# Kernel tuning notes

Hardware: AMD Instinct MI355X
Metric: run time of the kernel (lower is better)

## Reference

```python
import jax, jax.numpy as jnp
import numpy as np

N, E, C, S, G = 20000, 320000, 32, 64, 64
NRAD, HRAD, OUTS, HHEAD, NSH, NL = 8, 64, 16, 64, 9, 2
RCUT = 5.0
LIDX = np.repeat(np.arange(3), [1, 3, 5])  # l index of each of the 9 sh components


def _sph_harm(u):
    # real spherical harmonics up to l=2 on unit vectors, [E,3] -> [E,9]
    x, y, z = u[:, 0], u[:, 1], u[:, 2]
    s3 = jnp.sqrt(jnp.asarray(3.0, u.dtype))
    return jnp.stack([
        jnp.ones_like(x), x, y, z,
        s3 * x * y, s3 * y * z, 0.5 * (3 * z * z - 1.0), s3 * x * z,
        0.5 * s3 * (x * x - y * y)
    ], axis=1)


def _bessel(r):
    # Bessel radial basis with smooth polynomial envelope, [E] -> [E, NRAD]
    n = jnp.arange(1, NRAD + 1, dtype=r.dtype)
    rs = jnp.clip(r, 1e-6, None)[:, None]
    u = jnp.clip(r / RCUT, 0.0, 1.0)
    env = ((1 - u) ** 2 * (1 + 2 * u))[:, None]
    return jnp.sqrt(2.0 / RCUT) * jnp.sin(n * jnp.pi * rs / RCUT) / rs * env


def setup_inputs() -> dict:
    key = jax.random.key(0)
    ks = jax.random.split(key, 16)
    return {
        'vectors': jax.random.normal(ks[0], (E, 3), jnp.float32),
        'node_species': jax.random.randint(ks[1], (N,), 0, S),
        'senders': jax.random.randint(ks[2], (E,), 0, N),
        'receivers': jax.random.randint(ks[3], (E,), 0, N),
        'graph_id': jnp.sort(jax.random.randint(ks[4], (N,), 0, G)),
        'species_embed': jax.random.normal(ks[5], (S, C), jnp.float32) * 0.1,
        'w_r1': jax.random.normal(ks[6], (NRAD, HRAD), jnp.float32) / np.sqrt(NRAD),
        'b_r1': jnp.zeros((HRAD,), jnp.float32),
        'w_r2': jax.random.normal(ks[7], (NL, HRAD, 3 * C), jnp.float32) / np.sqrt(HRAD),
        'w_mix': jax.random.normal(ks[8], (NL, 3, C, C), jnp.float32) / np.sqrt(C),
        'w_sc': jax.random.normal(ks[9], (NL, S, C, C), jnp.float32) / np.sqrt(C),
        'w_readout': jax.random.normal(ks[10], (C, OUTS), jnp.float32) / np.sqrt(C),
        'ln_gamma': jnp.ones((OUTS,), jnp.float32),
        'ln_beta': jnp.zeros((OUTS,), jnp.float32),
        'w_h1': jax.random.normal(ks[11], (OUTS, HHEAD), jnp.float32) / np.sqrt(OUTS),
        'b_h1': jnp.zeros((HHEAD,), jnp.float32),
        'w_h2': jax.random.normal(ks[12], (HHEAD, 1), jnp.float32) / np.sqrt(HHEAD),
        'b_h2': jnp.zeros((1,), jnp.float32),
        'scale': jnp.ones((), jnp.float32),
        'shift': jnp.zeros((), jnp.float32),
    }


def reference(vectors, node_species, senders, receivers, graph_id, species_embed,
              w_r1, b_r1, w_r2, w_mix, w_sc, w_readout, ln_gamma, ln_beta,
              w_h1, b_h1, w_h2, b_h2, scale, shift):
    lidx = jnp.asarray(LIDX)
    # nan-safe edge norms and unit vectors (safe_norm in source)
    r2 = jnp.sum(vectors ** 2, axis=-1)
    r = jnp.where(r2 == 0, 0.0, jnp.sqrt(jnp.where(r2 == 0, 1.0, r2)))
    u = vectors / jnp.where(r == 0, 1.0, r)[:, None]
    sh = _sph_harm(u)                                  # [E,9]
    rad = jax.nn.silu(_bessel(r) @ w_r1 + b_r1)        # [E,HRAD] radial MLP
    h = species_embed[node_species]                    # [N,C] node embedding
    for li in range(NL):
        # per-edge, per-l, per-channel radial weights, expanded to the 9 sh components
        rw = (rad @ w_r2[li]).reshape(E, 3, C)[:, lidx, :]     # [E,9,C]
        # tensor-product message: radial * sender scalars * Y_lm
        msg = sh[:, :, None] * rw * h[senders][:, None, :]     # [E,9,C]
        agg = jax.ops.segment_sum(msg, receivers, num_segments=N)  # [N,9,C]
        # per-irrep (per-l) channel-mixing linear
        mixed = jnp.einsum('nmc,mcd->nmd', agg, w_mix[li][lidx])   # [N,9,C]
        # species-dependent self-connection on the scalar (l=0) channel
        sc = jnp.einsum('nc,ncd->nd', h, w_sc[li][node_species])   # [N,C]
        h = mixed[:, 0, :] + sc + h                                # residual
    readout = h @ w_readout                            # [N,OUTS] (last-block readout)
    mu = jnp.mean(readout, axis=-1, keepdims=True)
    var = jnp.var(readout, axis=-1, keepdims=True)
    nrm = (readout - mu) * jax.lax.rsqrt(var + 1e-6) * ln_gamma + ln_beta
    node_out = (jax.nn.gelu(nrm @ w_h1 + b_h1) @ w_h2 + b_h2)[:, 0]  # [N]
    gsum = jax.ops.segment_sum(node_out, graph_id, num_segments=G)
    cnt = jax.ops.segment_sum(jnp.ones((N,), node_out.dtype), graph_id, num_segments=G)
    gmean = gsum / jnp.clip(cnt, 1.0, None)            # segment-mean node2graph
    return (gmean * scale + shift)[:, None]            # [G,1]
```

## Files before the change

### kernel.cpp

```cpp
#include <hip/hip_runtime.h>
#include <hip/hip_fp16.h>
#include <cstdint>
#include <cmath>

#define NE 320000
#define NN 20000
#define NG 64

typedef __attribute__((ext_vector_type(8))) short s16x8;
typedef __attribute__((ext_vector_type(4))) float f32x4;

static __device__ __forceinline__ unsigned short f32_to_bf16(float x) {
    unsigned int u = __float_as_uint(x);
    u = (u + 0x7fffu + ((u >> 16) & 1u)) >> 16;
    return (unsigned short)u;
}
static __device__ __forceinline__ float bf16_to_f32(unsigned short h) {
    return __uint_as_float(((unsigned int)h) << 16);
}

__global__ __launch_bounds__(256) void setup_kernel(
    const int* __restrict__ spec, const float* __restrict__ emb,
    float* __restrict__ h,
    const float* __restrict__ w_r2,
    unsigned short* __restrict__ wt_hi, unsigned short* __restrict__ wt_lo,
    int* __restrict__ deg, float* __restrict__ gz)
{
    int t = blockIdx.x * 256 + threadIdx.x;
    if (t < NN * 32) h[t] = emb[spec[t >> 5] * 32 + (t & 31)];
    if (t < 4096) {
        int c = t >> 6, k = t & 63;
        float v = w_r2[(c >= 32 ? 6144 : 0) + k * 96 + (c & 31)];
        unsigned short hb = f32_to_bf16(v);
        wt_hi[t] = hb;
        wt_lo[t] = f32_to_bf16(v - bf16_to_f32(hb));
    }
    if (t < NN) deg[t] = 0;
    if (t < 128) gz[t] = 0.0f;
}

__global__ __launch_bounds__(256) void count_kernel(
    const int* __restrict__ recv, int* __restrict__ deg)
{
    int e = blockIdx.x * 256 + threadIdx.x;
    atomicAdd(&deg[recv[e]], 1);
}

__global__ __launch_bounds__(1024) void scan_kernel(
    const int* __restrict__ deg,
    int* __restrict__ rowstart, int* __restrict__ cursor)
{
    __shared__ int tsum[1024];
    const int tid = threadIdx.x;
    const int PER = (NN + 1023) / 1024;
    const int base = tid * PER;

    int s = 0;
    for (int i = 0; i < PER; ++i) {
        int idx = base + i;
        if (idx < NN) s += deg[idx];
    }
    tsum[tid] = s;
    __syncthreads();
    for (int off = 1; off < 1024; off <<= 1) {
        int v = (tid >= off) ? tsum[tid - off] : 0;
        __syncthreads();
        tsum[tid] += v;
        __syncthreads();
    }
    int run = tsum[tid] - s;
    for (int i = 0; i < PER; ++i) {
        int idx = base + i;
        if (idx < NN) {
            rowstart[idx] = run;
            cursor[idx] = run;
            run += deg[idx];
        }
    }
    if (tid == 1023) rowstart[NN] = NE;
}

__global__ __launch_bounds__(256) void scatter_kernel(
    const int* __restrict__ recv, const int* __restrict__ snd,
    int* __restrict__ cursor, int* __restrict__ eperm, int* __restrict__ esnd)
{
    int e = blockIdx.x * 256 + threadIdx.x;
    int slot = atomicAdd(&cursor[recv[e]], 1);
    eperm[e] = slot;
    esnd[slot] = snd[e];
}

__global__ __launch_bounds__(256) void edge_gemm_kernel(
    const float* __restrict__ vectors,
    const float* __restrict__ w_r1,
    const float* __restrict__ b_r1,
    const unsigned short* __restrict__ wt_hi,
    const unsigned short* __restrict__ wt_lo,
    const int* __restrict__ eperm,
    __half* __restrict__ rw0_0,
    __half* __restrict__ rw0_1)
{
    __shared__ __attribute__((aligned(16))) short sh_hi[256 * 72];
    __shared__ __attribute__((aligned(16))) short sh_lo[256 * 72];

    const int tid = threadIdx.x;
    const int e = blockIdx.x * 256 + tid;
    const int slot = eperm[e];

    float x = vectors[3 * e + 0];
    float y = vectors[3 * e + 1];
    float z = vectors[3 * e + 2];
    float r2 = x * x + y * y + z * z;
    float r = (r2 == 0.0f) ? 0.0f : sqrtf(r2);
    float rs = fmaxf(r, 1e-6f);
    float u = fminf(r * 0.2f, 1.0f);
    float env = (1.0f - u) * (1.0f - u) * (1.0f + 2.0f * u);
    float pref = 0.6324555320336759f * env / rs;
    float theta = 0.6283185307179586f * rs;

    float s1 = __sinf(theta), c1 = __cosf(theta);
    float twoc = 2.0f * c1;
    float b[8];
    {
        float sp = 0.0f, s = s1;
#pragma unroll
        for (int n = 0; n < 8; ++n) {
            b[n] = pref * s;
            float nx = twoc * s - sp;
            sp = s; s = nx;
        }
    }

#pragma unroll
    for (int j0 = 0; j0 < 64; j0 += 8) {
        short hibuf[8], lobuf[8];
#pragma unroll
        for (int jj = 0; jj < 8; ++jj) {
            int j = j0 + jj;
            float pre = b_r1[j];
#pragma unroll
            for (int n = 0; n < 8; ++n) pre = fmaf(b[n], w_r1[n * 64 + j], pre);
            float rj = pre * __builtin_amdgcn_rcpf(1.0f + __expf(-pre));
            unsigned short hb = f32_to_bf16(rj);
            float lov = rj - bf16_to_f32(hb);
            hibuf[jj] = (short)hb;
            lobuf[jj] = (short)f32_to_bf16(lov);
        }
        *(s16x8*)&sh_hi[tid * 72 + j0] =
            (s16x8){hibuf[0],hibuf[1],hibuf[2],hibuf[3],hibuf[4],hibuf[5],hibuf[6],hibuf[7]};
        *(s16x8*)&sh_lo[tid * 72 + j0] =
            (s16x8){lobuf[0],lobuf[1],lobuf[2],lobuf[3],lobuf[4],lobuf[5],lobuf[6],lobuf[7]};
    }

    __syncthreads();

    const int wv = tid >> 6;
    const int l = tid & 63;
    const int lrow = l & 15;
    const int lk = l >> 4;

    s16x8 Bhi[4][2], Blo[4][2];
#pragma unroll
    for (int ct = 0; ct < 4; ++ct)
#pragma unroll
        for (int kt = 0; kt < 2; ++kt) {
            int col = ct * 16 + lrow;
            int kof = kt * 32 + lk * 8;
            Bhi[ct][kt] = *(const s16x8*)(wt_hi + col * 64 + kof);
            Blo[ct][kt] = *(const s16x8*)(wt_lo + col * 64 + kof);
        }

    f32x4 acc[4][4];
#pragma unroll
    for (int rt = 0; rt < 4; ++rt)
#pragma unroll
        for (int ct = 0; ct < 4; ++ct) acc[rt][ct] = (f32x4){0.f, 0.f, 0.f, 0.f};

#pragma unroll
    for (int rt = 0; rt < 4; ++rt) {
        int row = wv * 64 + rt * 16 + lrow;
#pragma unroll
        for (int kt = 0; kt < 2; ++kt) {
            s16x8 ahi = *(const s16x8*)&sh_hi[row * 72 + kt * 32 + lk * 8];
            s16x8 alo = *(const s16x8*)&sh_lo[row * 72 + kt * 32 + lk * 8];
#pragma unroll
            for (int ct = 0; ct < 4; ++ct) {
                acc[rt][ct] = __builtin_amdgcn_mfma_f32_16x16x32_bf16(ahi, Bhi[ct][kt], acc[rt][ct], 0, 0, 0);
                acc[rt][ct] = __builtin_amdgcn_mfma_f32_16x16x32_bf16(alo, Bhi[ct][kt], acc[rt][ct], 0, 0, 0);
                acc[rt][ct] = __builtin_amdgcn_mfma_f32_16x16x32_bf16(ahi, Blo[ct][kt], acc[rt][ct], 0, 0, 0);
            }
        }
    }

    __syncthreads();
    __half* stg = (__half*)sh_hi;
#pragma unroll
    for (int rt = 0; rt < 4; ++rt)
#pragma unroll
        for (int ct = 0; ct < 4; ++ct) {
            int col = ct * 16 + lrow;
#pragma unroll
            for (int rr = 0; rr < 4; ++rr) {
                int erow = wv * 64 + rt * 16 + lk * 4 + rr;
                stg[erow * 72 + col] = __float2half_rn(acc[rt][ct][rr]);
            }
        }
    __syncthreads();
    {
        const s16x8* src = (const s16x8*)&sh_hi[tid * 72];
        size_t eb = (size_t)slot * 32;
        s16x8* d0 = (s16x8*)(rw0_0 + eb);
        s16x8* d1 = (s16x8*)(rw0_1 + eb);
        d0[0] = src[0]; d0[1] = src[1]; d0[2] = src[2]; d0[3] = src[3];
        d1[0] = src[4]; d1[1] = src[5]; d1[2] = src[6]; d1[3] = src[7];
    }
}

__device__ __forceinline__ float agg_update_val(
    const __half* __restrict__ rw0h, const float* __restrict__ hin,
    const int* __restrict__ rowstart, const int* __restrict__ esnd,
    const int* __restrict__ spec,
    const float* __restrict__ wmix0, const float* __restrict__ wscl,
    int t, int n, int c, int half)
{
    int s0 = rowstart[n], s1 = rowstart[n + 1];
    float hv = hin[t];

    float p0 = 0.f, p1 = 0.f, p2 = 0.f, p3 = 0.f;
    int k = s0;
    for (; k + 4 <= s1; k += 4) {
        int sA = esnd[k], sB = esnd[k + 1], sC = esnd[k + 2], sD = esnd[k + 3];
        float rA = __half2float(rw0h[(size_t)k * 32 + c]);
        float rB = __half2float(rw0h[(size_t)(k + 1) * 32 + c]);
        float rC = __half2float(rw0h[(size_t)(k + 2) * 32 + c]);
        float rD = __half2float(rw0h[(size_t)(k + 3) * 32 + c]);
        float hA = hin[(size_t)sA * 32 + c];
        float hB = hin[(size_t)sB * 32 + c];
        float hC = hin[(size_t)sC * 32 + c];
        float hD = hin[(size_t)sD * 32 + c];
        p0 = fmaf(rA, hA, p0);
        p1 = fmaf(rB, hB, p1);
        p2 = fmaf(rC, hC, p2);
        p3 = fmaf(rD, hD, p3);
    }
    for (; k < s1; ++k)
        p0 = fmaf(__half2float(rw0h[(size_t)k * 32 + c]),
                  hin[(size_t)esnd[k] * 32 + c], p0);
    float acc = (p0 + p1) + (p2 + p3);

    const float* wsc = wscl + spec[n] * 1024;
    float m0 = 0.f, m1 = 0.f, q0 = 0.f, q1 = 0.f;
#pragma unroll
    for (int cp = 0; cp < 32; cp += 2) {
        float av0 = __shfl(acc, half + cp);
        float hb0 = __shfl(hv, half + cp);
        float av1 = __shfl(acc, half + cp + 1);
        float hb1 = __shfl(hv, half + cp + 1);
        m0 = fmaf(av0, wmix0[cp * 32 + c], m0);
        q0 = fmaf(hb0, wsc[cp * 32 + c], q0);
        m1 = fmaf(av1, wmix0[(cp + 1) * 32 + c], m1);
        q1 = fmaf(hb1, wsc[(cp + 1) * 32 + c], q1);
    }
    return hv + (m0 + m1) + (q0 + q1);
}

__global__ __launch_bounds__(256) void agg_update_kernel(
    const __half* __restrict__ rw0h, const float* __restrict__ hin,
    const int* __restrict__ rowstart, const int* __restrict__ esnd,
    const int* __restrict__ spec,
    const float* __restrict__ wmix0, const float* __restrict__ wscl,
    float* __restrict__ hout)
{
    int t = blockIdx.x * 256 + threadIdx.x;
    int n = t >> 5, c = t & 31;
    int half = (threadIdx.x & 63) & 32;
    hout[t] = agg_update_val(rw0h, hin, rowstart, esnd, spec, wmix0, wscl,
                             t, n, c, half);
}

__global__ __launch_bounds__(256) void agg_readout_kernel(
    const __half* __restrict__ rw0h, const float* __restrict__ hin,
    const int* __restrict__ rowstart, const int* __restrict__ esnd,
    const int* __restrict__ spec,
    const float* __restrict__ wmix0, const float* __restrict__ wscl,
    const int* __restrict__ gid_arr,
    const float* __restrict__ w_ro,
    const float* __restrict__ gamma, const float* __restrict__ beta,
    const float* __restrict__ w_h1, const float* __restrict__ b_h1,
    const float* __restrict__ w_h2, const float* __restrict__ b_h2,
    float* __restrict__ gsum, float* __restrict__ gcnt)
{
    __shared__ int sgid[8];
    __shared__ float sval[8];

    int t = blockIdx.x * 256 + threadIdx.x;
    int n = t >> 5, c = t & 31;
    int half = (threadIdx.x & 63) & 32;

    float outv = agg_update_val(rw0h, hin, rowstart, esnd, spec, wmix0, wscl,
                                t, n, c, half);

    int o = c & 15;
    float r0 = 0.f, r1 = 0.f, r2 = 0.f, r3 = 0.f;
#pragma unroll
    for (int cp = 0; cp < 32; cp += 4) {
        r0 = fmaf(__shfl(outv, half + cp),     w_ro[cp * 16 + o],       r0);
        r1 = fmaf(__shfl(outv, half + cp + 1), w_ro[(cp + 1) * 16 + o], r1);
        r2 = fmaf(__shfl(outv, half + cp + 2), w_ro[(cp + 2) * 16 + o], r2);
        r3 = fmaf(__shfl(outv, half + cp + 3), w_ro[(cp + 3) * 16 + o], r3);
    }
    float ro = (r0 + r1) + (r2 + r3);

    float ssum = ro;
#pragma unroll
    for (int m = 1; m < 16; m <<= 1) ssum += __shfl_xor(ssum, m);
    float mu = ssum * (1.0f / 16.0f);
    float d = ro - mu;
    float vs = d * d;
#pragma unroll
    for (int m = 1; m < 16; m <<= 1) vs += __shfl_xor(vs, m);
    float inv = rsqrtf(vs * (1.0f / 16.0f) + 1e-6f);
    float nrm = d * inv * gamma[o] + beta[o];

    int j1 = c, j2 = c + 32;
    float a1a = b_h1[j1], a1b = 0.f, a2a = b_h1[j2], a2b = 0.f;
#pragma unroll
    for (int oo = 0; oo < 16; oo += 2) {
        float nv0 = __shfl(nrm, half + oo);
        float nv1 = __shfl(nrm, half + oo + 1);
        a1a = fmaf(nv0, w_h1[oo * 64 + j1], a1a);
        a2a = fmaf(nv0, w_h1[oo * 64 + j2], a2a);
        a1b = fmaf(nv1, w_h1[(oo + 1) * 64 + j1], a1b);
        a2b = fmaf(nv1, w_h1[(oo + 1) * 64 + j2], a2b);
    }
    float a1 = a1a + a1b, a2 = a2a + a2b;
    float g1 = 0.5f * a1 * (1.0f + tanhf(0.7978845608028654f * (a1 + 0.044715f * a1 * a1 * a1)));
    float g2 = 0.5f * a2 * (1.0f + tanhf(0.7978845608028654f * (a2 + 0.044715f * a2 * a2 * a2)));
    float partial = fmaf(g1, w_h2[j1], g2 * w_h2[j2]);
#pragma unroll
    for (int m = 1; m < 32; m <<= 1) partial += __shfl_xor(partial, m);

    if (c == 0) {
        int hw = threadIdx.x >> 5;
        sgid[hw] = gid_arr[n];
        sval[hw] = partial + b_h2[0];
    }
    __syncthreads();
    if (threadIdx.x == 0) {
        int g0 = sgid[0];
        float accv = sval[0];
        float cnt = 1.0f;
        for (int i = 1; i < 8; ++i) {
            if (sgid[i] == g0) { accv += sval[i]; cnt += 1.0f; }
            else {
                atomicAdd(&gsum[g0], accv);
                atomicAdd(&gcnt[g0], cnt);
                g0 = sgid[i]; accv = sval[i]; cnt = 1.0f;
            }
        }
        atomicAdd(&gsum[g0], accv);
        atomicAdd(&gcnt[g0], cnt);
    }
}

__global__ void finalize_kernel(const float* __restrict__ gsum,
                                const float* __restrict__ gcnt,
                                const float* __restrict__ scale,
                                const float* __restrict__ shift,
                                float* __restrict__ out)
{
    int g = threadIdx.x;
    if (g < NG) out[g] = gsum[g] / fmaxf(gcnt[g], 1.0f) * scale[0] + shift[0];
}

extern "C" void kernel_launch(void* const* d_in, const int* in_sizes, int n_in,
                              void* d_out, int out_size, void* d_ws, size_t ws_size,
                              hipStream_t stream)
{
    const float* vectors       = (const float*)d_in[0];
    const int*   node_species  = (const int*)d_in[1];
    const int*   senders       = (const int*)d_in[2];
    const int*   receivers     = (const int*)d_in[3];
    const int*   graph_id      = (const int*)d_in[4];
    const float* species_embed = (const float*)d_in[5];
    const float* w_r1          = (const float*)d_in[6];
    const float* b_r1          = (const float*)d_in[7];
    const float* w_r2          = (const float*)d_in[8];
    const float* w_mix         = (const float*)d_in[9];
    const float* w_sc          = (const float*)d_in[10];
    const float* w_ro          = (const float*)d_in[11];
    const float* ln_gamma      = (const float*)d_in[12];
    const float* ln_beta       = (const float*)d_in[13];
    const float* w_h1          = (const float*)d_in[14];
    const float* b_h1          = (const float*)d_in[15];
    const float* w_h2          = (const float*)d_in[16];
    const float* b_h2          = (const float*)d_in[17];
    const float* scale         = (const float*)d_in[18];
    const float* shift         = (const float*)d_in[19];
    float* out = (float*)d_out;

    __half* rw0_0 = (__half*)d_ws;
    __half* rw0_1 = rw0_0 + (size_t)NE * 32;
    float* hA     = (float*)(rw0_1 + (size_t)NE * 32);
    float* hB     = hA + (size_t)NN * 32;
    float* gsum   = hB + (size_t)NN * 32;
    float* gcnt   = gsum + NG;
    unsigned short* wt_hi = (unsigned short*)(gcnt + NG);
    unsigned short* wt_lo = wt_hi + 4096;
    int* deg      = (int*)(wt_lo + 4096);
    int* rowstart = deg + NN;
    int* cursor   = rowstart + NN + 1;
    int* eperm    = cursor + NN + 1;
    int* esnd     = eperm + NE;

    setup_kernel<<<(NN * 32 + 255) / 256, 256, 0, stream>>>(
        node_species, species_embed, hA, w_r2, wt_hi, wt_lo, deg, gsum);

    count_kernel<<<NE / 256, 256, 0, stream>>>(receivers, deg);

    scan_kernel<<<1, 1024, 0, stream>>>(deg, rowstart, cursor);

    scatter_kernel<<<NE / 256, 256, 0, stream>>>(receivers, senders, cursor, eperm, esnd);

    edge_gemm_kernel<<<NE / 256, 256, 0, stream>>>(
        vectors, w_r1, b_r1, wt_hi, wt_lo, eperm, rw0_0, rw0_1);

    agg_update_kernel<<<(NN * 32) / 256, 256, 0, stream>>>(
        rw0_0, hA, rowstart, esnd, node_species, w_mix, w_sc, hB);

    agg_readout_kernel<<<(NN * 32) / 256, 256, 0, stream>>>(
        rw0_1, hB, rowstart, esnd, node_species, w_mix + 3072, w_sc + 65536,
        graph_id, w_ro, ln_gamma, ln_beta, w_h1, b_h1, w_h2, b_h2, gsum, gcnt);

    finalize_kernel<<<1, 64, 0, stream>>>(gsum, gcnt, scale, shift, out);
}
```

Measured before the change: 174.7 us.

## Fuse count+scan and readout+finalize via last-block tickets; gather edge GEMM by slot

Merges the degree-count and prefix-scan kernels into one launch in which the last block to finish does the scan, found with an atomic ticket. Finalize is folded into the readout kernel the same way. The scatter now records an inverse permutation, so the edge GEMM runs in CSR slot order: it gathers the input vectors and writes its outputs contiguously. GELU's tanh form is rewritten through exp and a fast reciprocal. The aim is fewer launches and coalesced edge writes, at the cost of a single-block serial scan tail, scattered reads of the vectors, and a slight change in GELU accuracy.

```diff
diff --git a/kernel.cpp b/kernel.cpp
--- a/kernel.cpp
+++ b/kernel.cpp
@@ -21,13 +21,13 @@
 
 __global__ __launch_bounds__(256) void setup_kernel(
     const int* __restrict__ spec, const float* __restrict__ emb,
-    float* __restrict__ h,
+    float* __restrict__ hA,
     const float* __restrict__ w_r2,
     unsigned short* __restrict__ wt_hi, unsigned short* __restrict__ wt_lo,
-    int* __restrict__ deg, float* __restrict__ gz)
+    int* __restrict__ deg, float* __restrict__ gz, int* __restrict__ tickets)
 {
     int t = blockIdx.x * 256 + threadIdx.x;
-    if (t < NN * 32) h[t] = emb[spec[t >> 5] * 32 + (t & 31)];
+    if (t < NN * 32) hA[t] = emb[spec[t >> 5] * 32 + (t & 31)];
     if (t < 4096) {
         int c = t >> 6, k = t & 63;
         float v = w_r2[(c >= 32 ? 6144 : 0) + k * 96 + (c & 31)];
@@ -37,24 +37,27 @@
     }
     if (t < NN) deg[t] = 0;
     if (t < 128) gz[t] = 0.0f;
-}
-
-__global__ __launch_bounds__(256) void count_kernel(
-    const int* __restrict__ recv, int* __restrict__ deg)
-{
-    int e = blockIdx.x * 256 + threadIdx.x;
-    atomicAdd(&deg[recv[e]], 1);
-}
-
-__global__ __launch_bounds__(1024) void scan_kernel(
-    const int* __restrict__ deg,
-    int* __restrict__ rowstart, int* __restrict__ cursor)
-{
+    if (t < 2) tickets[t] = 0;
+}
+
+__global__ __launch_bounds__(1024) void count_scan_kernel(
+    const int* __restrict__ recv,
+    int* __restrict__ deg, int* __restrict__ rowstart, int* __restrict__ cursor,
+    int* __restrict__ ticket)
+{
+    __shared__ int is_last;
     __shared__ int tsum[1024];
     const int tid = threadIdx.x;
-    const int PER = (NN + 1023) / 1024;
+    int e = blockIdx.x * 1024 + tid;
+    if (e < NE) atomicAdd(&deg[recv[e]], 1);
+    __threadfence();
+    __syncthreads();
+    if (tid == 0) is_last = (atomicAdd(ticket, 1) == (int)gridDim.x - 1);
+    __syncthreads();
+    if (!is_last) return;
+
+    const int PER = 20;
     const int base = tid * PER;
-
     int s = 0;
     for (int i = 0; i < PER; ++i) {
         int idx = base + i;
@@ -82,11 +85,11 @@
 
 __global__ __launch_bounds__(256) void scatter_kernel(
     const int* __restrict__ recv, const int* __restrict__ snd,
-    int* __restrict__ cursor, int* __restrict__ eperm, int* __restrict__ esnd)
+    int* __restrict__ cursor, int* __restrict__ eidp, int* __restrict__ esnd)
 {
     int e = blockIdx.x * 256 + threadIdx.x;
     int slot = atomicAdd(&cursor[recv[e]], 1);
-    eperm[e] = slot;
+    eidp[slot] = e;
     esnd[slot] = snd[e];
 }
 
@@ -96,7 +99,7 @@
     const float* __restrict__ b_r1,
     const unsigned short* __restrict__ wt_hi,
     const unsigned short* __restrict__ wt_lo,
-    const int* __restrict__ eperm,
+    const int* __restrict__ eidp,
     __half* __restrict__ rw0_0,
     __half* __restrict__ rw0_1)
 {
@@ -104,8 +107,8 @@
     __shared__ __attribute__((aligned(16))) short sh_lo[256 * 72];
 
     const int tid = threadIdx.x;
-    const int e = blockIdx.x * 256 + tid;
-    const int slot = eperm[e];
+    const int slot = blockIdx.x * 256 + tid;
+    const int e = eidp[slot];
 
     float x = vectors[3 * e + 0];
     float y = vectors[3 * e + 1];
@@ -208,9 +211,9 @@
     __syncthreads();
     {
         const s16x8* src = (const s16x8*)&sh_hi[tid * 72];
-        size_t eb = (size_t)slot * 32;
-        s16x8* d0 = (s16x8*)(rw0_0 + eb);
-        s16x8* d1 = (s16x8*)(rw0_1 + eb);
+        size_t sb = (size_t)slot * 32;
+        s16x8* d0 = (s16x8*)(rw0_0 + sb);
+        s16x8* d1 = (s16x8*)(rw0_1 + sb);
         d0[0] = src[0]; d0[1] = src[1]; d0[2] = src[2]; d0[3] = src[3];
         d1[0] = src[4]; d1[1] = src[5]; d1[2] = src[6]; d1[3] = src[7];
     }
@@ -288,10 +291,14 @@
     const float* __restrict__ gamma, const float* __restrict__ beta,
     const float* __restrict__ w_h1, const float* __restrict__ b_h1,
     const float* __restrict__ w_h2, const float* __restrict__ b_h2,
-    float* __restrict__ gsum, float* __restrict__ gcnt)
+    float* __restrict__ gsum, float* __restrict__ gcnt,
+    int* __restrict__ ticket,
+    const float* __restrict__ scale, const float* __restrict__ shift,
+    float* __restrict__ out)
 {
     __shared__ int sgid[8];
     __shared__ float sval[8];
+    __shared__ int is_last;
 
     int t = blockIdx.x * 256 + threadIdx.x;
     int n = t >> 5, c = t & 31;
@@ -334,8 +341,10 @@
         a2b = fmaf(nv1, w_h1[(oo + 1) * 64 + j2], a2b);
     }
     float a1 = a1a + a1b, a2 = a2a + a2b;
-    float g1 = 0.5f * a1 * (1.0f + tanhf(0.7978845608028654f * (a1 + 0.044715f * a1 * a1 * a1)));
-    float g2 = 0.5f * a2 * (1.0f + tanhf(0.7978845608028654f * (a2 + 0.044715f * a2 * a2 * a2)));
+    float g1 = a1 * __builtin_amdgcn_rcpf(
+        1.0f + __expf(-1.5957691216057308f * (a1 + 0.044715f * a1 * a1 * a1)));
+    float g2 = a2 * __builtin_amdgcn_rcpf(
+        1.0f + __expf(-1.5957691216057308f * (a2 + 0.044715f * a2 * a2 * a2)));
     float partial = fmaf(g1, w_h2[j1], g2 * w_h2[j2]);
 #pragma unroll
     for (int m = 1; m < 32; m <<= 1) partial += __shfl_xor(partial, m);
@@ -361,16 +370,16 @@
         atomicAdd(&gsum[g0], accv);
         atomicAdd(&gcnt[g0], cnt);
     }
-}
-
-__global__ void finalize_kernel(const float* __restrict__ gsum,
-                                const float* __restrict__ gcnt,
-                                const float* __restrict__ scale,
-                                const float* __restrict__ shift,
-                                float* __restrict__ out)
-{
-    int g = threadIdx.x;
-    if (g < NG) out[g] = gsum[g] / fmaxf(gcnt[g], 1.0f) * scale[0] + shift[0];
+
+    __threadfence();
+    __syncthreads();
+    if (threadIdx.x == 0) is_last = (atomicAdd(ticket, 1) == (int)gridDim.x - 1);
+    __syncthreads();
+    if (is_last && threadIdx.x < NG) {
+        float gs = atomicAdd(&gsum[threadIdx.x], 0.0f);
+        float gc = atomicAdd(&gcnt[threadIdx.x], 0.0f);
+        out[threadIdx.x] = gs / fmaxf(gc, 1.0f) * scale[0] + shift[0];
+    }
 }
 
 extern "C" void kernel_launch(void* const* d_in, const int* in_sizes, int n_in,
@@ -410,27 +419,27 @@
     int* deg      = (int*)(wt_lo + 4096);
     int* rowstart = deg + NN;
     int* cursor   = rowstart + NN + 1;
-    int* eperm    = cursor + NN + 1;
-    int* esnd     = eperm + NE;
+    int* eidp     = cursor + NN + 1;
+    int* esnd     = eidp + NE;
+    int* tickets  = esnd + NE;
 
     setup_kernel<<<(NN * 32 + 255) / 256, 256, 0, stream>>>(
-        node_species, species_embed, hA, w_r2, wt_hi, wt_lo, deg, gsum);
-
-    count_kernel<<<NE / 256, 256, 0, stream>>>(receivers, deg);
-
-    scan_kernel<<<1, 1024, 0, stream>>>(deg, rowstart, cursor);
-
-    scatter_kernel<<<NE / 256, 256, 0, stream>>>(receivers, senders, cursor, eperm, esnd);
+        node_species, species_embed, hA, w_r2, wt_hi, wt_lo, deg, gsum, tickets);
+
+    count_scan_kernel<<<(NE + 1023) / 1024, 1024, 0, stream>>>(
+        receivers, deg, rowstart, cursor, tickets);
+
+    scatter_kernel<<<NE / 256, 256, 0, stream>>>(
+        receivers, senders, cursor, eidp, esnd);
 
     edge_gemm_kernel<<<NE / 256, 256, 0, stream>>>(
-        vectors, w_r1, b_r1, wt_hi, wt_lo, eperm, rw0_0, rw0_1);
+        vectors, w_r1, b_r1, wt_hi, wt_lo, eidp, rw0_0, rw0_1);
 
     agg_update_kernel<<<(NN * 32) / 256, 256, 0, stream>>>(
         rw0_0, hA, rowstart, esnd, node_species, w_mix, w_sc, hB);
 
     agg_readout_kernel<<<(NN * 32) / 256, 256, 0, stream>>>(
         rw0_1, hB, rowstart, esnd, node_species, w_mix + 3072, w_sc + 65536,
-        graph_id, w_ro, ln_gamma, ln_beta, w_h1, b_h1, w_h2, b_h2, gsum, gcnt);
-
-    finalize_kernel<<<1, 64, 0, stream>>>(gsum, gcnt, scale, shift, out);
-}
+        graph_id, w_ro, ln_gamma, ln_beta, w_h1, b_h1, w_h2, b_h2,
+        gsum, gcnt, tickets + 1, scale, shift, out);
+}
```

Result: slower. 383.3 us (+119.5%).
